# Performance work log

Measured on AMD Instinct MI355X. Metric: run time of the kernel, lower is better.

## Reference

```python
import jax, jax.numpy as jnp
import numpy as np

N = 50000        # nodes
E = 1_600_000    # edges
D_IN = 128       # input_dim
H = 2            # n_heads
C = 32           # out_dim per head


def setup_inputs() -> dict:
    key = jax.random.key(0)
    ks = jax.random.split(key, 10)
    x = jax.random.normal(ks[0], (N, D_IN), dtype=jnp.float32)
    edge_index = jax.random.randint(ks[1], (2, E), 0, N, dtype=jnp.int64)
    s = 1.0 / np.sqrt(D_IN)
    Wq = jax.random.uniform(ks[2], (D_IN, H * C), jnp.float32, -s, s)
    bq = jax.random.uniform(ks[3], (H * C,), jnp.float32, -s, s)
    Wk = jax.random.uniform(ks[4], (D_IN, H * C), jnp.float32, -s, s)
    bk = jax.random.uniform(ks[5], (H * C,), jnp.float32, -s, s)
    Wv = jax.random.uniform(ks[6], (D_IN, H * C), jnp.float32, -s, s)
    bv = jax.random.uniform(ks[7], (H * C,), jnp.float32, -s, s)
    Wskip = jax.random.uniform(ks[8], (D_IN, H * C), jnp.float32, -s, s)
    bskip = jax.random.uniform(ks[9], (H * C,), jnp.float32, -s, s)
    return {"x": x, "edge_index": edge_index, "Wq": Wq, "bq": bq,
            "Wk": Wk, "bk": bk, "Wv": Wv, "bv": bv,
            "Wskip": Wskip, "bskip": bskip}


def reference(x, edge_index, Wq, bq, Wk, bk, Wv, bv, Wskip, bskip):
    # IntraGraphAttention.forward: ELU then TransformerConv (PyG semantics,
    # concat=True, root_weight=True, beta=False).
    x = jax.nn.elu(x)
    src, dst = edge_index[0], edge_index[1]

    q = (x @ Wq + bq).reshape(N, H, C)   # queries at target nodes
    k = (x @ Wk + bk).reshape(N, H, C)   # keys at source nodes
    v = (x @ Wv + bv).reshape(N, H, C)   # values at source nodes

    # per-edge attention logits [E, H]
    alpha = jnp.einsum('ehc,ehc->eh', q[dst], k[src]) / np.sqrt(C).astype(np.float32)

    # segment softmax over incoming edges of each target node
    m = jax.ops.segment_max(alpha, dst, num_segments=N)            # [N, H]
    m = jnp.where(jnp.isfinite(m), m, 0.0)                          # empty segments
    ex = jnp.exp(alpha - m[dst])                                    # [E, H]
    denom = jax.ops.segment_sum(ex, dst, num_segments=N)            # [N, H]
    w = ex / jnp.maximum(denom[dst], 1e-16)                         # [E, H]

    # weighted scatter-add of values to targets
    msg = v[src] * w[:, :, None]                                    # [E, H, C]
    out = jax.ops.segment_sum(msg, dst, num_segments=N)             # [N, H, C]
    out = out.reshape(N, H * C)

    # root/skip connection
    return out + x @ Wskip + bskip
```

## Files before the change

### kernel.cpp

```cpp
#include <hip/hip_runtime.h>
#include <hip/hip_bf16.h>


#define DIN 128
#define HC  64
#define EPB 4096
#define CAPB 12288

typedef _Float16 h2 __attribute__((ext_vector_type(2)));
typedef _Float16 h4 __attribute__((ext_vector_type(4)));
typedef _Float16 h8 __attribute__((ext_vector_type(8)));
typedef float    f4 __attribute__((ext_vector_type(4)));

#if defined(__has_builtin)
#if __has_builtin(__builtin_amdgcn_fdot2)
#define HAVE_FDOT2 1
#endif
#endif

static __device__ __forceinline__ float fdot2(h2 a, h2 b, float c) {
#ifdef HAVE_FDOT2
    return __builtin_amdgcn_fdot2(a, b, c, false);
#else
    return fmaf((float)a.x, (float)b.x, fmaf((float)a.y, (float)b.y, c));
#endif
}

union h2i { h2 h; int i; };
static __device__ __forceinline__ h2 shfl_xor_h2(h2 v, int m) {
    h2i u; u.h = v;
    u.i = __shfl_xor(u.i, m, 64);
    return u.h;
}

__global__ __launch_bounds__(256) void k_prep(
        const float* __restrict__ Wq, const float* __restrict__ Wk,
        const float* __restrict__ Wv, const float* __restrict__ Ws,
        _Float16* __restrict__ Wh, int* __restrict__ bucketCnt) {
    int t = threadIdx.x;
    if (blockIdx.x == 0) bucketCnt[t] = 0;
    int idx = blockIdx.x * 256 + t;
    int m    = idx >> 13;
    int rem  = idx & 8191;
    int grp  = rem >> 9;
    int ks   = grp >> 2;
    int nt   = grp & 3;
    int r3   = rem & 511;
    int lane = r3 >> 3;
    int j    = r3 & 7;
    int k = ks * 32 + (lane >> 4) * 8 + j;
    int n = nt * 16 + (lane & 15);
    const float* W = (m == 0) ? Wq : (m == 1) ? Wk : (m == 2) ? Wv : Ws;
    Wh[idx] = (_Float16)W[k * 64 + n];
}

#define TB 32
#define XS 136
__global__ __launch_bounds__(256) void k_fused(
        const float4* __restrict__ x4,
        const _Float16* __restrict__ Wh,
        const float* __restrict__ bq, const float* __restrict__ bk,
        const float* __restrict__ bv, const float* __restrict__ bs,
        _Float16* __restrict__ Q, _Float16* __restrict__ K, _Float16* __restrict__ V,
        float* __restrict__ OUT, int N,
        const int* __restrict__ ei, int* __restrict__ bucketCnt,
        unsigned int* __restrict__ part, int E, int qb) {
    __shared__ alignas(16) char smem[4096 + EPB * 4];
    int t = threadIdx.x;

    if ((int)blockIdx.x >= qb) {
        int* hist  = (int*)smem;
        int* lbase = hist + 256;
        int* cur   = lbase + 256;
        int* gbase = cur + 256;
        unsigned int* stg = (unsigned int*)(smem + 4096);

        int e0 = (blockIdx.x - qb) * EPB;
        int cnt = min(EPB, E - e0);
        hist[t] = 0; cur[t] = 0;
        __syncthreads();

        unsigned int pk[EPB / 256];
        #pragma unroll
        for (int u = 0; u < EPB / 256; ++u) {
            int i = t + u * 256;
            if (i < cnt) {
                unsigned int d = (unsigned int)ei[E + e0 + i];
                unsigned int s = (unsigned int)ei[e0 + i];
                pk[u] = (d << 16) | s;
                atomicAdd(&hist[d >> 8], 1);
            }
        }
        __syncthreads();
        {
            int v = hist[t];
            lbase[t] = v;
            __syncthreads();
            for (int off = 1; off < 256; off <<= 1) {
                int xv = (t >= off) ? lbase[t - off] : 0;
                __syncthreads();
                lbase[t] += xv;
                __syncthreads();
            }
            int incl = lbase[t];
            __syncthreads();
            lbase[t] = incl - v;
        }
        {
            int c = hist[t];
            if (c > 0) gbase[t] = t * CAPB + atomicAdd(&bucketCnt[t], c);
        }
        __syncthreads();
        #pragma unroll
        for (int u = 0; u < EPB / 256; ++u) {
            int i = t + u * 256;
            if (i < cnt) {
                int b = pk[u] >> 24;
                int r = atomicAdd(&cur[b], 1);
                stg[lbase[b] + r] = pk[u];
            }
        }
        __syncthreads();
        for (int i = t; i < cnt; i += 256) {
            unsigned int pkv = stg[i];
            int b = pkv >> 24;
            part[gbase[b] + (i - lbase[b])] = pkv;
        }
        return;
    }

    _Float16* xs = (_Float16*)smem;
    int n0 = blockIdx.x * TB;

    #pragma unroll
    for (int u = 0; u < 4; ++u) {
        int idx = t + u * 256;
        int row = idx >> 5;
        int k4  = idx & 31;
        int node = n0 + row;
        float4 v = make_float4(0.f, 0.f, 0.f, 0.f);
        if (node < N) v = x4[(size_t)node * 32 + k4];
        v.x = (v.x > 0.f) ? v.x : expm1f(v.x);
        v.y = (v.y > 0.f) ? v.y : expm1f(v.y);
        v.z = (v.z > 0.f) ? v.z : expm1f(v.z);
        v.w = (v.w > 0.f) ? v.w : expm1f(v.w);
        h4 hv = { (_Float16)v.x, (_Float16)v.y, (_Float16)v.z, (_Float16)v.w };
        *(h4*)&xs[row * XS + k4 * 4] = hv;
    }
    __syncthreads();

    int m    = t >> 6;
    int lane = t & 63;
    int lr   = lane & 15;
    int lq   = lane >> 4;

    const _Float16* Wm = Wh + m * 8192;
    const float* bias = (m == 0) ? bq : (m == 1) ? bk : (m == 2) ? bv : bs;

    f4 acc[2][4];
    #pragma unroll
    for (int mt = 0; mt < 2; ++mt)
        #pragma unroll
        for (int nt = 0; nt < 4; ++nt)
            acc[mt][nt] = (f4){0.f, 0.f, 0.f, 0.f};

    #pragma unroll
    for (int ks = 0; ks < 4; ++ks) {
        h8 a0 = *(const h8*)&xs[lr * XS + ks * 32 + lq * 8];
        h8 a1 = *(const h8*)&xs[(16 + lr) * XS + ks * 32 + lq * 8];
        #pragma unroll
        for (int nt = 0; nt < 4; ++nt) {
            h8 b = *(const h8*)&Wm[((ks * 4 + nt) << 9) + lane * 8];
            acc[0][nt] = __builtin_amdgcn_mfma_f32_16x16x32_f16(a0, b, acc[0][nt], 0, 0, 0);
            acc[1][nt] = __builtin_amdgcn_mfma_f32_16x16x32_f16(a1, b, acc[1][nt], 0, 0, 0);
        }
    }

    _Float16* Om = (m == 0) ? Q : (m == 1) ? K : V;
    #pragma unroll
    for (int nt = 0; nt < 4; ++nt) {
        int col = nt * 16 + lr;
        float bb = bias[col];
        #pragma unroll
        for (int mt = 0; mt < 2; ++mt) {
            #pragma unroll
            for (int r = 0; r < 4; ++r) {
                int node = n0 + mt * 16 + lq * 4 + r;
                if (node < N) {
                    float val = acc[mt][nt][r] + bb;
                    if (m == 3) OUT[((size_t)node << 6) + col] = val;
                    else        Om[((size_t)node << 6) + col] = (_Float16)val;
                }
            }
        }
    }
}

__global__ __launch_bounds__(512) void k_build(
        const unsigned int* __restrict__ part, const int* __restrict__ bucketCnt,
        unsigned short* __restrict__ srcs16, int* __restrict__ row_ptr,
        int N, int NBK, int E) {
    __shared__ int hist[256], basep[256], cur[256], sd[256];
    __shared__ unsigned short sbuf[CAPB];
    __shared__ int s_outBase, s_cnt;
    int t = threadIdx.x;
    int b = blockIdx.x;

    int bc = (t < NBK) ? bucketCnt[t] : 0;
    if (t < 256) sd[t] = bc;
    __syncthreads();
    for (int off = 1; off < 256; off <<= 1) {
        int xv = (t >= off && t < 256) ? sd[t - off] : 0;
        __syncthreads();
        if (t < 256) sd[t] += xv;
        __syncthreads();
    }
    if (t == b) { s_outBase = sd[t] - bc; s_cnt = bc; }
    if (b == 0 && t == 256) row_ptr[N] = E;
    if (t < 256) { hist[t] = 0; cur[t] = 0; }
    __syncthreads();
    int outBase = s_outBase;
    int cnt = s_cnt;
    int s0 = b * CAPB;

    for (int i = t; i < cnt; i += 512) {
        unsigned int pkv = part[s0 + i];
        atomicAdd(&hist[(pkv >> 16) & 255], 1);
    }
    __syncthreads();
    {
        int v = (t < 256) ? hist[t] : 0;
        if (t < 256) sd[t] = v;
        __syncthreads();
        for (int off = 1; off < 256; off <<= 1) {
            int xv = (t >= off && t < 256) ? sd[t - off] : 0;
            __syncthreads();
            if (t < 256) sd[t] += xv;
            __syncthreads();
        }
        if (t < 256) basep[t] = sd[t] - v;
    }
    __syncthreads();

    if (cnt <= CAPB) {
        for (int i = t; i < cnt; i += 512) {
            unsigned int pkv = part[s0 + i];
            int d = (pkv >> 16) & 255;
            int r = atomicAdd(&cur[d], 1);
            sbuf[basep[d] + r] = (unsigned short)(pkv & 0xFFFFu);
        }
        __syncthreads();
        for (int i = t; i < cnt; i += 512) srcs16[outBase + i] = sbuf[i];
    } else {
        for (int i = t; i < cnt; i += 512) {
            unsigned int pkv = part[s0 + i];
            int d = (pkv >> 16) & 255;
            int r = atomicAdd(&cur[d], 1);
            srcs16[outBase + basep[d] + r] = (unsigned short)(pkv & 0xFFFFu);
        }
    }

    int node = (b << 8) + t;
    if (t < 256 && node < N) row_ptr[node] = outBase + basep[t];
}

__global__ __launch_bounds__(256) void k_attn(
        const _Float16* __restrict__ Q, const _Float16* __restrict__ K,
        const _Float16* __restrict__ V, const int* __restrict__ row_ptr,
        const unsigned short* __restrict__ srcs16, float* __restrict__ out, int N) {
    int lane = threadIdx.x & 63;
    int wave = threadIdx.x >> 6;
    int n = blockIdx.x * 4 + wave;
    if (n >= N) return;
    int h5 = lane & 32;
    int c  = lane & 31;
    int es = (lane >> 3) & 3;
    int cq = lane & 7;

    int start = row_ptr[n];
    int deg   = row_ptr[n + 1] - start;
    if (deg <= 0) return;

    h8 q8[4];
    {
        const h8* qp = (const h8*)(Q + ((size_t)n << 6) + h5);
        #pragma unroll
        for (int r = 0; r < 4; ++r) q8[r] = qp[r];
    }

    const float scale = 0.17677669529663687f;
    float lsum = 0.f;
    h2 acc01 = (h2){(_Float16)0.f, (_Float16)0.f};
    h2 acc23 = (h2){(_Float16)0.f, (_Float16)0.f};

    for (int i0 = 0; i0 < deg; i0 += 32) {
        int nb = min(32, deg - i0);
        int sc = 0;
        if (c < nb) sc = (int)srcs16[start + i0 + c];

        const h8* kp = (const h8*)(K + ((size_t)sc << 6) + h5);
        float s = 0.f;
        #pragma unroll
        for (int r = 0; r < 4; ++r) {
            h8 kv = kp[r];
            const h2* k2 = (const h2*)&kv;
            const h2* q2 = (const h2*)&q8[r];
            s = fdot2(k2[0], q2[0], s);
            s = fdot2(k2[1], q2[1], s);
            s = fdot2(k2[2], q2[2], s);
            s = fdot2(k2[3], q2[3], s);
        }
        float ex = (c < nb) ? __expf(s * scale) : 0.f;
        lsum += ex;

        int nbp = (nb + 3) & ~3;
        for (int j0 = 0; j0 < nbp; j0 += 4) {
            int j = j0 + es;
            float w  = __shfl(ex, h5 + j, 64);
            int   sj = __shfl(sc, h5 + j, 64);
            h4 vv = *(const h4*)(V + ((size_t)sj << 6) + h5 + (cq << 2));
            _Float16 wh = (_Float16)w;
            h2 w2 = (h2){wh, wh};
            acc01 += w2 * (h2){vv[0], vv[1]};
            acc23 += w2 * (h2){vv[2], vv[3]};
        }
    }

    acc01 += shfl_xor_h2(acc01, 8);
    acc23 += shfl_xor_h2(acc23, 8);
    acc01 += shfl_xor_h2(acc01, 16);
    acc23 += shfl_xor_h2(acc23, 16);

    float ls = lsum;
    ls += __shfl_xor(ls, 16, 64);
    ls += __shfl_xor(ls,  8, 64);
    ls += __shfl_xor(ls,  4, 64);
    ls += __shfl_xor(ls,  2, 64);
    ls += __shfl_xor(ls,  1, 64);
    float rden = 1.0f / fmaxf(ls, 1e-16f);

    if ((lane & 24) == 0) {
        float* o = out + ((size_t)n << 6) + h5 + (cq << 2);
        float4 cur4 = *(float4*)o;
        cur4.x += (float)acc01[0] * rden;
        cur4.y += (float)acc01[1] * rden;
        cur4.z += (float)acc23[0] * rden;
        cur4.w += (float)acc23[1] * rden;
        *(float4*)o = cur4;
    }
}

extern "C" void kernel_launch(void* const* d_in, const int* in_sizes, int n_in,
                              void* d_out, int out_size, void* d_ws, size_t ws_size,
                              hipStream_t stream) {
    const float* x  = (const float*)d_in[0];
    const int*   ei = (const int*)d_in[1];
    const float* Wq = (const float*)d_in[2];
    const float* bq = (const float*)d_in[3];
    const float* Wk = (const float*)d_in[4];
    const float* bk = (const float*)d_in[5];
    const float* Wv = (const float*)d_in[6];
    const float* bv = (const float*)d_in[7];
    const float* Ws = (const float*)d_in[8];
    const float* bs = (const float*)d_in[9];
    float* out = (float*)d_out;

    int N = in_sizes[0] / DIN;
    int E = in_sizes[1] / 2;
    int NBK = (N + 255) >> 8;

    char* ws = (char*)d_ws;
    size_t off = 0;
    auto carve = [&](size_t bytes) -> void* {
        void* p = ws + off;
        off = (off + bytes + 255) & ~(size_t)255;
        return p;
    };
    int*            bucketCnt = (int*)carve(256 * sizeof(int));
    int*            row_ptr   = (int*)carve((size_t)(N + 1) * sizeof(int));
    unsigned int*   part      = (unsigned int*)carve((size_t)NBK * CAPB * sizeof(unsigned int));
    unsigned short* srcs16    = (unsigned short*)carve((size_t)E * sizeof(unsigned short));
    _Float16*       Wh        = (_Float16*)carve(4 * 8192 * sizeof(_Float16));
    _Float16*       Qh        = (_Float16*)carve((size_t)N * HC * sizeof(_Float16));
    _Float16*       Kh        = (_Float16*)carve((size_t)N * HC * sizeof(_Float16));
    _Float16*       Vh        = (_Float16*)carve((size_t)N * HC * sizeof(_Float16));
    (void)ws_size; (void)n_in; (void)out_size;

    int qb = (N + TB - 1) / TB;
    int cb = (E + EPB - 1) / EPB;

    k_prep<<<128, 256, 0, stream>>>(Wq, Wk, Wv, Ws, Wh, bucketCnt);
    k_fused<<<qb + cb, 256, 0, stream>>>(
        (const float4*)x, Wh, bq, bk, bv, bs,
        Qh, Kh, Vh, out, N,
        ei, bucketCnt, part, E, qb);
    k_build<<<NBK, 512, 0, stream>>>(part, bucketCnt, srcs16, row_ptr, N, NBK, E);
    k_attn<<<(N + 3) / 4, 256, 0, stream>>>(Qh, Kh, Vh, row_ptr, srcs16, out, N);
}
```

Baseline: 193.0 us.

## Restructure attention value aggregation to two edges per pass with fp32 accumulators

The value-gather loop changes from four edges per iteration with 4-wide fp16 loads to two edges per pass, each lane loading an h2 of V and accumulating in fp32. The loop body is unrolled four times per group of eight edges, so each lane handles more edges per lane-column and the cross-lane reduction at the end shrinks to one shuffle step. The next chunk's source indices are prefetched before the dot products to hide index-load latency. Accumulating in fp32 improves accuracy, but the narrower loads mean more load instructions overall.

```diff
diff --git a/kernel.cpp b/kernel.cpp
--- a/kernel.cpp
+++ b/kernel.cpp
@@ -24,13 +24,6 @@
 #else
     return fmaf((float)a.x, (float)b.x, fmaf((float)a.y, (float)b.y, c));
 #endif
-}
-
-union h2i { h2 h; int i; };
-static __device__ __forceinline__ h2 shfl_xor_h2(h2 v, int m) {
-    h2i u; u.h = v;
-    u.i = __shfl_xor(u.i, m, 64);
-    return u.h;
 }
 
 __global__ __launch_bounds__(256) void k_prep(
@@ -274,8 +267,8 @@
     if (n >= N) return;
     int h5 = lane & 32;
     int c  = lane & 31;
-    int es = (lane >> 3) & 3;
-    int cq = lane & 7;
+    int pairHalf = (lane >> 4) & 1;
+    int clg = (h5 >> 1) + (lane & 15);
 
     int start = row_ptr[n];
     int deg   = row_ptr[n + 1] - start;
@@ -290,46 +283,58 @@
 
     const float scale = 0.17677669529663687f;
     float lsum = 0.f;
-    h2 acc01 = (h2){(_Float16)0.f, (_Float16)0.f};
-    h2 acc23 = (h2){(_Float16)0.f, (_Float16)0.f};
+    float2 acc2 = make_float2(0.f, 0.f);
+
+    int sc_next = (c < deg) ? (int)srcs16[start + c] : 0;
 
     for (int i0 = 0; i0 < deg; i0 += 32) {
         int nb = min(32, deg - i0);
-        int sc = 0;
-        if (c < nb) sc = (int)srcs16[start + i0 + c];
+        int sc = sc_next;
 
         const h8* kp = (const h8*)(K + ((size_t)sc << 6) + h5);
+        h8 kv0 = kp[0], kv1 = kp[1], kv2 = kp[2], kv3 = kp[3];
+
+        int i1 = i0 + 32;
+        if (i1 < deg) {
+            sc_next = (c < deg - i1) ? (int)srcs16[start + i1 + c] : 0;
+        }
+
         float s = 0.f;
-        #pragma unroll
-        for (int r = 0; r < 4; ++r) {
-            h8 kv = kp[r];
-            const h2* k2 = (const h2*)&kv;
-            const h2* q2 = (const h2*)&q8[r];
-            s = fdot2(k2[0], q2[0], s);
-            s = fdot2(k2[1], q2[1], s);
-            s = fdot2(k2[2], q2[2], s);
-            s = fdot2(k2[3], q2[3], s);
+        {
+            const h2* q2;
+            const h2* k2;
+            k2 = (const h2*)&kv0; q2 = (const h2*)&q8[0];
+            s = fdot2(k2[0], q2[0], s); s = fdot2(k2[1], q2[1], s);
+            s = fdot2(k2[2], q2[2], s); s = fdot2(k2[3], q2[3], s);
+            k2 = (const h2*)&kv1; q2 = (const h2*)&q8[1];
+            s = fdot2(k2[0], q2[0], s); s = fdot2(k2[1], q2[1], s);
+            s = fdot2(k2[2], q2[2], s); s = fdot2(k2[3], q2[3], s);
+            k2 = (const h2*)&kv2; q2 = (const h2*)&q8[2];
+            s = fdot2(k2[0], q2[0], s); s = fdot2(k2[1], q2[1], s);
+            s = fdot2(k2[2], q2[2], s); s = fdot2(k2[3], q2[3], s);
+            k2 = (const h2*)&kv3; q2 = (const h2*)&q8[3];
+            s = fdot2(k2[0], q2[0], s); s = fdot2(k2[1], q2[1], s);
+            s = fdot2(k2[2], q2[2], s); s = fdot2(k2[3], q2[3], s);
         }
         float ex = (c < nb) ? __expf(s * scale) : 0.f;
         lsum += ex;
 
-        int nbp = (nb + 3) & ~3;
-        for (int j0 = 0; j0 < nbp; j0 += 4) {
-            int j = j0 + es;
-            float w  = __shfl(ex, h5 + j, 64);
-            int   sj = __shfl(sc, h5 + j, 64);
-            h4 vv = *(const h4*)(V + ((size_t)sj << 6) + h5 + (cq << 2));
-            _Float16 wh = (_Float16)w;
-            h2 w2 = (h2){wh, wh};
-            acc01 += w2 * (h2){vv[0], vv[1]};
-            acc23 += w2 * (h2){vv[2], vv[3]};
-        }
-    }
-
-    acc01 += shfl_xor_h2(acc01, 8);
-    acc23 += shfl_xor_h2(acc23, 8);
-    acc01 += shfl_xor_h2(acc01, 16);
-    acc23 += shfl_xor_h2(acc23, 16);
+        int nbp = (nb + 7) & ~7;
+        for (int j0 = 0; j0 < nbp; j0 += 8) {
+            #pragma unroll
+            for (int u = 0; u < 4; ++u) {
+                int j = j0 + 2 * u + pairHalf;
+                float w  = __shfl(ex, h5 + j, 64);
+                int   sj = __shfl(sc, h5 + j, 64);
+                h2 vv = *(const h2*)(V + ((size_t)sj << 6) + (clg << 1));
+                acc2.x = fmaf(w, (float)vv.x, acc2.x);
+                acc2.y = fmaf(w, (float)vv.y, acc2.y);
+            }
+        }
+    }
+
+    acc2.x += __shfl_xor(acc2.x, 16, 64);
+    acc2.y += __shfl_xor(acc2.y, 16, 64);
 
     float ls = lsum;
     ls += __shfl_xor(ls, 16, 64);
@@ -339,14 +344,12 @@
     ls += __shfl_xor(ls,  1, 64);
     float rden = 1.0f / fmaxf(ls, 1e-16f);
 
-    if ((lane & 24) == 0) {
-        float* o = out + ((size_t)n << 6) + h5 + (cq << 2);
-        float4 cur4 = *(float4*)o;
-        cur4.x += (float)acc01[0] * rden;
-        cur4.y += (float)acc01[1] * rden;
-        cur4.z += (float)acc23[0] * rden;
-        cur4.w += (float)acc23[1] * rden;
-        *(float4*)o = cur4;
+    if ((lane & 16) == 0) {
+        float2* o2 = (float2*)out + ((size_t)n << 5) + clg;
+        float2 cur2 = *o2;
+        cur2.x += acc2.x * rden;
+        cur2.y += acc2.y * rden;
+        *o2 = cur2;
     }
 }
 
```

Result: faster. 188.9 us (-2.1%).
